# Performance work log

Hardware: AMD Instinct MI355X
Metric: run time of the kernel (lower is better)

The kernel has to match this reference:

```python
import jax, jax.numpy as jnp
import numpy as np
from jax import lax

B, T1, T2, C = 8, 128, 128, 256
K = 3

def setup_inputs() -> dict:
    key = jax.random.key(0)
    k1, k2, kw, kb = jax.random.split(key, 4)
    x1 = jax.random.normal(k1, (B, T1, C), dtype=jnp.float32)
    x2 = jax.random.normal(k2, (B, T2, C), dtype=jnp.float32)
    # conv2d: in_channels = 2C, out_channels = C, kernel 3x3 (OIHW)
    fan_in = 2 * C * K * K
    bound = 1.0 / np.sqrt(fan_in)
    W = jax.random.uniform(kw, (C, 2 * C, K, K), jnp.float32, -bound, bound)
    b = jax.random.uniform(kb, (C,), jnp.float32, -bound, bound)
    alpha = jnp.float32(0.5)
    return {"x1": x1, "x2": x2, "W": W, "b": b, "alpha": alpha}


def reference(x1, x2, W, b, alpha):
    # x1: [B, T1, C], x2: [B, T2, C]
    a = jnp.transpose(x1, (0, 2, 1))  # [B, C, T1]
    c2 = jnp.transpose(x2, (0, 2, 1))  # [B, C, T2]
    Bd, Cd, T1d = a.shape
    T2d = c2.shape[-1]
    # joint outer-product tensor: [B, 2C, T1, T2]
    j1 = jnp.broadcast_to(a[:, :, :, None], (Bd, Cd, T1d, T2d))
    j2 = jnp.broadcast_to(c2[:, :, None, :], (Bd, Cd, T1d, T2d))
    joint = jnp.concatenate([j1, j2], axis=1)
    out = lax.conv_general_dilated(
        joint, W, window_strides=(1, 1), padding="SAME",
        dimension_numbers=("NCHW", "OIHW", "NCHW"))
    out = out + b[None, :, None, None]
    out = jax.nn.gelu(out, approximate=False)  # torch nn.GELU default = exact erf
    out_T1 = jnp.mean(out, axis=-1)            # [B, C, T1]
    out_T1 = jnp.transpose(out_T1, (0, 2, 1))  # [B, T1, C]
    return out_T1 * alpha + x1
```

## Files before the change

### kernel.cpp

```cpp
#include <hip/hip_runtime.h>
#include <math.h>

#define B_   8
#define T_   128
#define C_   256
#define M_   1024
#define NO   2304
#define LDP  136

typedef unsigned short ushort;
typedef ushort ushort8v __attribute__((ext_vector_type(8)));
typedef __bf16 bf16x8  __attribute__((ext_vector_type(8)));
typedef float  f32x4   __attribute__((ext_vector_type(4)));

__device__ __forceinline__ ushort f2bf(float f) {
    unsigned u = __float_as_uint(f);
    u += 0x7fffu + ((u >> 16) & 1u);
    return (ushort)(u >> 16);
}

__device__ __forceinline__ float gelu_fast(float x) {
    float x2 = x * x;
    float y  = x * fmaf(0.0713548162726f, x2, 1.59576912161f);
    float e  = __expf(-y);
    return x * __builtin_amdgcn_rcpf(1.0f + e);
}

__device__ __forceinline__ ushort8v pack8(float4 lo, float4 hi) {
    ushort8v u;
    u[0] = f2bf(lo.x); u[1] = f2bf(lo.y); u[2] = f2bf(lo.z); u[3] = f2bf(lo.w);
    u[4] = f2bf(hi.x); u[5] = f2bf(hi.y); u[6] = f2bf(hi.z); u[7] = f2bf(hi.w);
    return u;
}

__global__ __launch_bounds__(256) void tc_pack_w(
    const float* __restrict__ W, ushort* __restrict__ Wt)
{
    const int o = blockIdx.x, t = threadIdx.x;
    __shared__ ushort lw[4608];
    const float* src = W + (size_t)o * 4608;
    #pragma unroll
    for (int i = 0; i < 18; ++i)
        lw[t + i * 256] = f2bf(src[t + i * 256]);
    __syncthreads();
    #pragma unroll
    for (int i = 0; i < 18; ++i) {
        int e   = t + i * 256;
        int row = e >> 8;
        int c   = e & 255;
        int s   = (row >= 9);
        int r   = row - s * 9;
        Wt[((size_t)s * NO + o * 9 + r) * C_ + c] = lw[((s << 8) + c) * 9 + r];
    }
}

__global__ __launch_bounds__(256) void tc_gemm(
    const float* __restrict__ x1, const float* __restrict__ x2,
    const ushort* __restrict__ Wt, float* __restrict__ G)
{
    const int tn = blockIdx.x;
    const int tm = blockIdx.y;
    const int s  = blockIdx.z;

    __shared__ ushort As[64 * LDP];
    __shared__ ushort Bs[64 * LDP];

    const int tid = threadIdx.x;
    const int r   = tid & 63;
    const int q   = tid >> 6;

    const float*  Xr = (s ? x2 : x1) + ((size_t)(tm * 64 + r)) * C_ + q * 32;
    const ushort* Wr = Wt + ((size_t)s * NO + tn * 64 + r) * C_ + q * 32;

    float4 al0[8], al1[8];
    ushort8v bl0[4], bl1[4];
    #pragma unroll
    for (int i = 0; i < 8; ++i) al0[i] = *(const float4*)(Xr + i * 4);
    #pragma unroll
    for (int i = 0; i < 4; ++i) bl0[i] = *(const ushort8v*)(Wr + i * 8);
    #pragma unroll
    for (int i = 0; i < 8; ++i) al1[i] = *(const float4*)(Xr + 128 + i * 4);
    #pragma unroll
    for (int i = 0; i < 4; ++i) bl1[i] = *(const ushort8v*)(Wr + 128 + i * 8);

    const int st = r * LDP + q * 32;
    #pragma unroll
    for (int c = 0; c < 4; ++c) {
        *(ushort8v*)&As[st + c * 8] = pack8(al0[2 * c], al0[2 * c + 1]);
        *(ushort8v*)&Bs[st + c * 8] = bl0[c];
    }
    __syncthreads();

    const int wr  = q >> 1, wc = q & 1;
    const int r16 = tid & 15, kb = (tid & 63) >> 4;
    const int ar  = (wr * 32 + r16) * LDP + kb * 8;
    const int br  = (wc * 32 + r16) * LDP + kb * 8;

    f32x4 acc[2][2] = {};
    #pragma unroll
    for (int ks = 0; ks < 4; ++ks) {
        bf16x8 a0 = __builtin_bit_cast(bf16x8, *(const ushort8v*)&As[ar + ks * 32]);
        bf16x8 a1 = __builtin_bit_cast(bf16x8, *(const ushort8v*)&As[ar + 16 * LDP + ks * 32]);
        bf16x8 b0 = __builtin_bit_cast(bf16x8, *(const ushort8v*)&Bs[br + ks * 32]);
        bf16x8 b1 = __builtin_bit_cast(bf16x8, *(const ushort8v*)&Bs[br + 16 * LDP + ks * 32]);
        acc[0][0] = __builtin_amdgcn_mfma_f32_16x16x32_bf16(a0, b0, acc[0][0], 0, 0, 0);
        acc[0][1] = __builtin_amdgcn_mfma_f32_16x16x32_bf16(a0, b1, acc[0][1], 0, 0, 0);
        acc[1][0] = __builtin_amdgcn_mfma_f32_16x16x32_bf16(a1, b0, acc[1][0], 0, 0, 0);
        acc[1][1] = __builtin_amdgcn_mfma_f32_16x16x32_bf16(a1, b1, acc[1][1], 0, 0, 0);
    }
    __syncthreads();

    #pragma unroll
    for (int c = 0; c < 4; ++c) {
        *(ushort8v*)&As[st + c * 8] = pack8(al1[2 * c], al1[2 * c + 1]);
        *(ushort8v*)&Bs[st + c * 8] = bl1[c];
    }
    __syncthreads();

    #pragma unroll
    for (int ks = 0; ks < 4; ++ks) {
        bf16x8 a0 = __builtin_bit_cast(bf16x8, *(const ushort8v*)&As[ar + ks * 32]);
        bf16x8 a1 = __builtin_bit_cast(bf16x8, *(const ushort8v*)&As[ar + 16 * LDP + ks * 32]);
        bf16x8 b0 = __builtin_bit_cast(bf16x8, *(const ushort8v*)&Bs[br + ks * 32]);
        bf16x8 b1 = __builtin_bit_cast(bf16x8, *(const ushort8v*)&Bs[br + 16 * LDP + ks * 32]);
        acc[0][0] = __builtin_amdgcn_mfma_f32_16x16x32_bf16(a0, b0, acc[0][0], 0, 0, 0);
        acc[0][1] = __builtin_amdgcn_mfma_f32_16x16x32_bf16(a0, b1, acc[0][1], 0, 0, 0);
        acc[1][0] = __builtin_amdgcn_mfma_f32_16x16x32_bf16(a1, b0, acc[1][0], 0, 0, 0);
        acc[1][1] = __builtin_amdgcn_mfma_f32_16x16x32_bf16(a1, b1, acc[1][1], 0, 0, 0);
    }

    #pragma unroll
    for (int j = 0; j < 2; ++j) {
        int n = tn * 64 + wc * 32 + j * 16 + r16;
        #pragma unroll
        for (int i = 0; i < 2; ++i) {
            int m = tm * 64 + wr * 32 + i * 16 + kb * 4;
            *(f32x4*)&G[((size_t)s * NO + n) * M_ + m] = acc[i][j];
        }
    }
}

__global__ __launch_bounds__(128) void tc_finalize(
    const float* __restrict__ G, const float* __restrict__ x1,
    const float* __restrict__ bias, const float* __restrict__ alpha_p,
    float* __restrict__ out)
{
    const int o = blockIdx.x & 255;
    const int b = blockIdx.x >> 8;
    const int t = threadIdx.x;

    __shared__ float Bs3[T_], BsT[T_], BsB[T_];

    const float* G0 = G + ((size_t)o * 9) * M_ + b * T_;
    const float* G1 = G + ((size_t)NO + o * 9) * M_ + b * T_;

    float a[3] = {0.f, 0.f, 0.f};
    #pragma unroll
    for (int kh = 0; kh < 3; ++kh) {
        int tm = t + kh - 1;
        if (tm >= 0 && tm < T_) {
            #pragma unroll
            for (int kw = 0; kw < 3; ++kw)
                a[kw] += G0[(kh * 3 + kw) * M_ + tm];
        }
    }
    float bb[3] = {0.f, 0.f, 0.f};
    #pragma unroll
    for (int kw = 0; kw < 3; ++kw) {
        int tm = t + kw - 1;
        if (tm >= 0 && tm < T_) {
            #pragma unroll
            for (int kh = 0; kh < 3; ++kh)
                bb[kh] += G1[(kh * 3 + kw) * M_ + tm];
        }
    }

    Bs3[t] = bb[0] + bb[1] + bb[2];
    BsT[t] = bb[1] + bb[2];
    BsB[t] = bb[0] + bb[1];

    float bo = bias[o];
    float A3 = bo + a[0] + a[1] + a[2];
    float Al = bo + a[1] + a[2];
    float Ar = bo + a[0] + a[1];

    __syncthreads();

    const float* Bsel = (t == 0) ? BsT : ((t == T_ - 1) ? BsB : Bs3);

    float s0 = 0.f, s1 = 0.f, s2 = 0.f, s3 = 0.f;
    for (int j = 0; j < T_; j += 4) {
        s0 += gelu_fast(A3 + Bsel[j]);
        s1 += gelu_fast(A3 + Bsel[j + 1]);
        s2 += gelu_fast(A3 + Bsel[j + 2]);
        s3 += gelu_fast(A3 + Bsel[j + 3]);
    }
    float sacc = (s0 + s1) + (s2 + s3);
    sacc += gelu_fast(Al + Bsel[0])      - gelu_fast(A3 + Bsel[0]);
    sacc += gelu_fast(Ar + Bsel[T_ - 1]) - gelu_fast(A3 + Bsel[T_ - 1]);

    float alpha = *alpha_p;
    size_t oi = ((size_t)b * T_ + t) * C_ + o;
    out[oi] = sacc * (alpha * (1.0f / (float)T_)) + x1[oi];
}

extern "C" void kernel_launch(void* const* d_in, const int* in_sizes, int n_in,
                              void* d_out, int out_size, void* d_ws, size_t ws_size,
                              hipStream_t stream) {
    const float* x1    = (const float*)d_in[0];
    const float* x2    = (const float*)d_in[1];
    const float* W     = (const float*)d_in[2];
    const float* bias  = (const float*)d_in[3];
    const float* alpha = (const float*)d_in[4];
    float* out = (float*)d_out;

    float*  G  = (float*)d_ws;
    ushort* Wt = (ushort*)((char*)d_ws + (size_t)2 * NO * M_ * 4);

    tc_pack_w<<<256, 256, 0, stream>>>(W, Wt);
    tc_gemm<<<dim3(NO / 64, M_ / 64, 2), 256, 0, stream>>>(x1, x2, Wt, G);
    tc_finalize<<<B_ * C_, T_, 0, stream>>>(G, x1, bias, alpha, out);
}
```

Baseline: 104.6 us.

## Fuse GEMM and GELU-mean finalize into one kernel, pre-pack inputs to bf16

Replaces the three-kernel pipeline (pack W, GEMM writing a large fp32 G buffer, finalize) with two kernels. The first packs W and converts x1/x2 to bf16. The second runs, per batch and 8-output-channel group, the MFMA GEMM over both halves with register double-buffered loads, stages results as bf16 in LDS, and does the shifted sums, GELU row-mean and residual in place. This removes the global G round trip and one launch, at the cost of storing intermediates in bf16 and a grid of only 256 blocks of 512 threads. GELU now uses exp2 with pre-scaled constants.

```diff
diff --git a/kernel.cpp b/kernel.cpp
--- a/kernel.cpp
+++ b/kernel.cpp
@@ -4,204 +4,242 @@
 #define B_   8
 #define T_   128
 #define C_   256
-#define M_   1024
-#define NO   2304
-#define LDP  136
+#define XLDP 136
+#define SLDP 82
+
+#define OFF_WS 34816
+#define OFF_S1 20992
+#define OFF_BV 41984
+#define OFF_LO 54272
+#define SMEMB  58880
 
 typedef unsigned short ushort;
 typedef ushort ushort8v __attribute__((ext_vector_type(8)));
 typedef __bf16 bf16x8  __attribute__((ext_vector_type(8)));
 typedef float  f32x4   __attribute__((ext_vector_type(4)));
+typedef float  f32x2   __attribute__((ext_vector_type(2)));
 
 __device__ __forceinline__ ushort f2bf(float f) {
     unsigned u = __float_as_uint(f);
     u += 0x7fffu + ((u >> 16) & 1u);
     return (ushort)(u >> 16);
 }
+__device__ __forceinline__ float bf2f(ushort u) {
+    return __uint_as_float((unsigned)u << 16);
+}
 
 __device__ __forceinline__ float gelu_fast(float x) {
     float x2 = x * x;
-    float y  = x * fmaf(0.0713548162726f, x2, 1.59576912161f);
-    float e  = __expf(-y);
+    float y2 = x * fmaf(0.10294324f, x2, 2.3022082f);
+    float e  = exp2f(-y2);
     return x * __builtin_amdgcn_rcpf(1.0f + e);
 }
 
-__device__ __forceinline__ ushort8v pack8(float4 lo, float4 hi) {
-    ushort8v u;
-    u[0] = f2bf(lo.x); u[1] = f2bf(lo.y); u[2] = f2bf(lo.z); u[3] = f2bf(lo.w);
-    u[4] = f2bf(hi.x); u[5] = f2bf(hi.y); u[6] = f2bf(hi.z); u[7] = f2bf(hi.w);
-    return u;
-}
-
-__global__ __launch_bounds__(256) void tc_pack_w(
-    const float* __restrict__ W, ushort* __restrict__ Wt)
+__global__ __launch_bounds__(256) void tc_pack(
+    const float* __restrict__ x1, const float* __restrict__ x2,
+    const float* __restrict__ W, ushort* __restrict__ Xp,
+    ushort* __restrict__ Wt)
 {
-    const int o = blockIdx.x, t = threadIdx.x;
-    __shared__ ushort lw[4608];
-    const float* src = W + (size_t)o * 4608;
-    #pragma unroll
-    for (int i = 0; i < 18; ++i)
-        lw[t + i * 256] = f2bf(src[t + i * 256]);
-    __syncthreads();
-    #pragma unroll
-    for (int i = 0; i < 18; ++i) {
-        int e   = t + i * 256;
-        int row = e >> 8;
-        int c   = e & 255;
-        int s   = (row >= 9);
-        int r   = row - s * 9;
-        Wt[((size_t)s * NO + o * 9 + r) * C_ + c] = lw[((s << 8) + c) * 9 + r];
-    }
-}
-
-__global__ __launch_bounds__(256) void tc_gemm(
-    const float* __restrict__ x1, const float* __restrict__ x2,
-    const ushort* __restrict__ Wt, float* __restrict__ G)
+    const int bid = blockIdx.x, t = threadIdx.x;
+    if (bid < 256) {
+        __shared__ ushort lw[4608];
+        const float* src = W + (size_t)bid * 4608;
+        #pragma unroll
+        for (int i = 0; i < 18; ++i)
+            lw[t + i * 256] = f2bf(src[t + i * 256]);
+        __syncthreads();
+        #pragma unroll
+        for (int i = 0; i < 18; ++i) {
+            int d = t + i * 256;
+            int c = d & 255;
+            int row18 = d >> 8;
+            int s = (row18 >= 9) ? 1 : 0;
+            int r = row18 - s * 9;
+            int rsrc = (s == 0) ? r : ((r % 3) * 3 + (r / 3));
+            Wt[(((size_t)s * 256 + bid) * 9 + r) * 256 + c] = lw[(s * 256 + c) * 9 + rsrc];
+        }
+    } else {
+        int g = (bid - 256) * 256 + t;
+        int e = g * 8;
+        int s  = e >> 18;
+        int me = e & 262143;
+        int m  = me >> 8, c = me & 255;
+        const float* src = (s ? x2 : x1) + (size_t)m * 256 + c;
+        float4 lo = *(const float4*)src;
+        float4 hi = *(const float4*)(src + 4);
+        ushort8v u;
+        u[0] = f2bf(lo.x); u[1] = f2bf(lo.y); u[2] = f2bf(lo.z); u[3] = f2bf(lo.w);
+        u[4] = f2bf(hi.x); u[5] = f2bf(hi.y); u[6] = f2bf(hi.z); u[7] = f2bf(hi.w);
+        *(ushort8v*)&Xp[e] = u;
+    }
+}
+
+__global__ __launch_bounds__(512) void tc_fused(
+    const ushort* __restrict__ Xp, const ushort* __restrict__ Wt,
+    const float* __restrict__ x1, const float* __restrict__ bias,
+    const float* __restrict__ alpha_p, float* __restrict__ out)
 {
-    const int tn = blockIdx.x;
-    const int tm = blockIdx.y;
-    const int s  = blockIdx.z;
-
-    __shared__ ushort As[64 * LDP];
-    __shared__ ushort Bs[64 * LDP];
-
-    const int tid = threadIdx.x;
-    const int r   = tid & 63;
-    const int q   = tid >> 6;
-
-    const float*  Xr = (s ? x2 : x1) + ((size_t)(tm * 64 + r)) * C_ + q * 32;
-    const ushort* Wr = Wt + ((size_t)s * NO + tn * 64 + r) * C_ + q * 32;
-
-    float4 al0[8], al1[8];
-    ushort8v bl0[4], bl1[4];
-    #pragma unroll
-    for (int i = 0; i < 8; ++i) al0[i] = *(const float4*)(Xr + i * 4);
-    #pragma unroll
-    for (int i = 0; i < 4; ++i) bl0[i] = *(const ushort8v*)(Wr + i * 8);
-    #pragma unroll
-    for (int i = 0; i < 8; ++i) al1[i] = *(const float4*)(Xr + 128 + i * 4);
-    #pragma unroll
-    for (int i = 0; i < 4; ++i) bl1[i] = *(const ushort8v*)(Wr + 128 + i * 8);
-
-    const int st = r * LDP + q * 32;
-    #pragma unroll
-    for (int c = 0; c < 4; ++c) {
-        *(ushort8v*)&As[st + c * 8] = pack8(al0[2 * c], al0[2 * c + 1]);
-        *(ushort8v*)&Bs[st + c * 8] = bl0[c];
-    }
-    __syncthreads();
-
-    const int wr  = q >> 1, wc = q & 1;
-    const int r16 = tid & 15, kb = (tid & 63) >> 4;
-    const int ar  = (wr * 32 + r16) * LDP + kb * 8;
-    const int br  = (wc * 32 + r16) * LDP + kb * 8;
-
-    f32x4 acc[2][2] = {};
-    #pragma unroll
-    for (int ks = 0; ks < 4; ++ks) {
-        bf16x8 a0 = __builtin_bit_cast(bf16x8, *(const ushort8v*)&As[ar + ks * 32]);
-        bf16x8 a1 = __builtin_bit_cast(bf16x8, *(const ushort8v*)&As[ar + 16 * LDP + ks * 32]);
-        bf16x8 b0 = __builtin_bit_cast(bf16x8, *(const ushort8v*)&Bs[br + ks * 32]);
-        bf16x8 b1 = __builtin_bit_cast(bf16x8, *(const ushort8v*)&Bs[br + 16 * LDP + ks * 32]);
-        acc[0][0] = __builtin_amdgcn_mfma_f32_16x16x32_bf16(a0, b0, acc[0][0], 0, 0, 0);
-        acc[0][1] = __builtin_amdgcn_mfma_f32_16x16x32_bf16(a0, b1, acc[0][1], 0, 0, 0);
-        acc[1][0] = __builtin_amdgcn_mfma_f32_16x16x32_bf16(a1, b0, acc[1][0], 0, 0, 0);
-        acc[1][1] = __builtin_amdgcn_mfma_f32_16x16x32_bf16(a1, b1, acc[1][1], 0, 0, 0);
-    }
-    __syncthreads();
-
-    #pragma unroll
-    for (int c = 0; c < 4; ++c) {
-        *(ushort8v*)&As[st + c * 8] = pack8(al1[2 * c], al1[2 * c + 1]);
-        *(ushort8v*)&Bs[st + c * 8] = bl1[c];
-    }
-    __syncthreads();
-
-    #pragma unroll
-    for (int ks = 0; ks < 4; ++ks) {
-        bf16x8 a0 = __builtin_bit_cast(bf16x8, *(const ushort8v*)&As[ar + ks * 32]);
-        bf16x8 a1 = __builtin_bit_cast(bf16x8, *(const ushort8v*)&As[ar + 16 * LDP + ks * 32]);
-        bf16x8 b0 = __builtin_bit_cast(bf16x8, *(const ushort8v*)&Bs[br + ks * 32]);
-        bf16x8 b1 = __builtin_bit_cast(bf16x8, *(const ushort8v*)&Bs[br + 16 * LDP + ks * 32]);
-        acc[0][0] = __builtin_amdgcn_mfma_f32_16x16x32_bf16(a0, b0, acc[0][0], 0, 0, 0);
-        acc[0][1] = __builtin_amdgcn_mfma_f32_16x16x32_bf16(a0, b1, acc[0][1], 0, 0, 0);
-        acc[1][0] = __builtin_amdgcn_mfma_f32_16x16x32_bf16(a1, b0, acc[1][0], 0, 0, 0);
-        acc[1][1] = __builtin_amdgcn_mfma_f32_16x16x32_bf16(a1, b1, acc[1][1], 0, 0, 0);
-    }
-
-    #pragma unroll
-    for (int j = 0; j < 2; ++j) {
-        int n = tn * 64 + wc * 32 + j * 16 + r16;
-        #pragma unroll
-        for (int i = 0; i < 2; ++i) {
-            int m = tm * 64 + wr * 32 + i * 16 + kb * 4;
-            *(f32x4*)&G[((size_t)s * NO + n) * M_ + m] = acc[i][j];
-        }
-    }
-}
-
-__global__ __launch_bounds__(128) void tc_finalize(
-    const float* __restrict__ G, const float* __restrict__ x1,
-    const float* __restrict__ bias, const float* __restrict__ alpha_p,
-    float* __restrict__ out)
-{
-    const int o = blockIdx.x & 255;
-    const int b = blockIdx.x >> 8;
-    const int t = threadIdx.x;
-
-    __shared__ float Bs3[T_], BsT[T_], BsB[T_];
-
-    const float* G0 = G + ((size_t)o * 9) * M_ + b * T_;
-    const float* G1 = G + ((size_t)NO + o * 9) * M_ + b * T_;
-
-    float a[3] = {0.f, 0.f, 0.f};
-    #pragma unroll
-    for (int kh = 0; kh < 3; ++kh) {
-        int tm = t + kh - 1;
-        if (tm >= 0 && tm < T_) {
+    __shared__ __align__(16) char smem[SMEMB];
+    ushort* Xs = (ushort*)smem;
+    ushort* Ws = (ushort*)(smem + OFF_WS);
+    float*  Bv = (float*)(smem + OFF_BV);
+    float*  Lo = (float*)(smem + OFF_LO);
+
+    const int u  = threadIdx.x;
+    const int b  = blockIdx.x >> 5;
+    const int og = blockIdx.x & 31;
+    const int l  = u & 63, w = u >> 6;
+    const int r16 = l & 15, kb = l >> 4;
+
+    const int xrow = u >> 2, xcb = (u & 3) * 32;
+    const ushort* Xrow0 = Xp + ((size_t)(b * T_ + xrow)) * C_ + xcb;
+    const ushort* WtB   = Wt + ((size_t)og * 72) * C_;
+
+    f32x4 acc[2][5] = {};
+    ushort8v xbuf[2][4];
+    ushort8v wbuf[2][3];
+
+    #pragma unroll
+    for (int c4 = 0; c4 < 4; ++c4) xbuf[0][c4] = *(const ushort8v*)(Xrow0 + c4 * 8);
+    {
+        int c0 = u;          int r0 = c0 >> 4, o0 = (c0 & 15) * 8;
+        int c1 = 512 + u;    int r1 = c1 >> 4, o1 = (c1 & 15) * 8;
+        wbuf[0][0] = *(const ushort8v*)(WtB + (size_t)r0 * C_ + o0);
+        wbuf[0][1] = *(const ushort8v*)(WtB + (size_t)r1 * C_ + o1);
+        if (u < 128) {
+            int c2 = 1024 + u; int r2 = c2 >> 4, o2 = (c2 & 15) * 8;
+            wbuf[0][2] = *(const ushort8v*)(WtB + (size_t)r2 * C_ + o2);
+        }
+    }
+
+    #pragma unroll
+    for (int r = 0; r < 4; ++r) {
+        const int cur = r & 1;
+        __syncthreads();
+        #pragma unroll
+        for (int c4 = 0; c4 < 4; ++c4)
+            *(ushort8v*)&Xs[xrow * XLDP + xcb + c4 * 8] = xbuf[cur][c4];
+        {
+            int c0 = u;       *(ushort8v*)&Ws[(c0 >> 4) * XLDP + (c0 & 15) * 8] = wbuf[cur][0];
+            int c1 = 512 + u; *(ushort8v*)&Ws[(c1 >> 4) * XLDP + (c1 & 15) * 8] = wbuf[cur][1];
+            if (u < 128) {
+                int c2 = 1024 + u;
+                *(ushort8v*)&Ws[(c2 >> 4) * XLDP + (c2 & 15) * 8] = wbuf[cur][2];
+            }
+        }
+        if (r < 3) {
+            const int rn = r + 1, sn = rn >> 1, pn = rn & 1;
+            const ushort* xsrc = Xrow0 + (size_t)sn * 262144 + pn * 128;
             #pragma unroll
-            for (int kw = 0; kw < 3; ++kw)
-                a[kw] += G0[(kh * 3 + kw) * M_ + tm];
-        }
-    }
-    float bb[3] = {0.f, 0.f, 0.f};
-    #pragma unroll
-    for (int kw = 0; kw < 3; ++kw) {
-        int tm = t + kw - 1;
-        if (tm >= 0 && tm < T_) {
+            for (int c4 = 0; c4 < 4; ++c4)
+                xbuf[cur ^ 1][c4] = *(const ushort8v*)(xsrc + c4 * 8);
+            const ushort* wsrc = WtB + (size_t)sn * 2304 * C_ + pn * 128;
+            int c0 = u;       wbuf[cur ^ 1][0] = *(const ushort8v*)(wsrc + (size_t)(c0 >> 4) * C_ + (c0 & 15) * 8);
+            int c1 = 512 + u; wbuf[cur ^ 1][1] = *(const ushort8v*)(wsrc + (size_t)(c1 >> 4) * C_ + (c1 & 15) * 8);
+            if (u < 128) {
+                int c2 = 1024 + u;
+                wbuf[cur ^ 1][2] = *(const ushort8v*)(wsrc + (size_t)(c2 >> 4) * C_ + (c2 & 15) * 8);
+            }
+        }
+        __syncthreads();
+        const int s = r >> 1;
+        #pragma unroll
+        for (int ks = 0; ks < 4; ++ks) {
+            bf16x8 af = __builtin_bit_cast(bf16x8,
+                *(const ushort8v*)&Xs[(w * 16 + r16) * XLDP + ks * 32 + kb * 8]);
             #pragma unroll
-            for (int kh = 0; kh < 3; ++kh)
-                bb[kh] += G1[(kh * 3 + kw) * M_ + tm];
-        }
-    }
-
-    Bs3[t] = bb[0] + bb[1] + bb[2];
-    BsT[t] = bb[1] + bb[2];
-    BsB[t] = bb[0] + bb[1];
-
-    float bo = bias[o];
-    float A3 = bo + a[0] + a[1] + a[2];
-    float Al = bo + a[1] + a[2];
-    float Ar = bo + a[0] + a[1];
-
-    __syncthreads();
-
-    const float* Bsel = (t == 0) ? BsT : ((t == T_ - 1) ? BsB : Bs3);
-
-    float s0 = 0.f, s1 = 0.f, s2 = 0.f, s3 = 0.f;
-    for (int j = 0; j < T_; j += 4) {
-        s0 += gelu_fast(A3 + Bsel[j]);
-        s1 += gelu_fast(A3 + Bsel[j + 1]);
-        s2 += gelu_fast(A3 + Bsel[j + 2]);
-        s3 += gelu_fast(A3 + Bsel[j + 3]);
-    }
-    float sacc = (s0 + s1) + (s2 + s3);
-    sacc += gelu_fast(Al + Bsel[0])      - gelu_fast(A3 + Bsel[0]);
-    sacc += gelu_fast(Ar + Bsel[T_ - 1]) - gelu_fast(A3 + Bsel[T_ - 1]);
-
-    float alpha = *alpha_p;
-    size_t oi = ((size_t)b * T_ + t) * C_ + o;
-    out[oi] = sacc * (alpha * (1.0f / (float)T_)) + x1[oi];
+            for (int nf = 0; nf < 5; ++nf) {
+                bf16x8 bf = __builtin_bit_cast(bf16x8,
+                    *(const ushort8v*)&Ws[(nf * 16 + r16) * XLDP + ks * 32 + kb * 8]);
+                acc[s][nf] = __builtin_amdgcn_mfma_f32_16x16x32_bf16(af, bf, acc[s][nf], 0, 0, 0);
+            }
+        }
+    }
+    __syncthreads();
+
+    #pragma unroll
+    for (int s = 0; s < 2; ++s) {
+        ushort* Sb = (ushort*)(smem + (s ? OFF_S1 : 0));
+        #pragma unroll
+        for (int nf = 0; nf < 5; ++nf) {
+            int n = nf * 16 + r16;
+            if (n < 72) {
+                #pragma unroll
+                for (int reg = 0; reg < 4; ++reg) {
+                    int m = w * 16 + kb * 4 + reg;
+                    Sb[m * SLDP + n] = f2bf(acc[s][nf][reg]);
+                }
+            }
+        }
+    }
+    __syncthreads();
+
+    const int oo  = w;
+    const int t0  = l;
+    const int o_g = og * 8 + oo;
+    const float bo = bias[o_g];
+    const ushort* S0 = (const ushort*)smem;
+    const ushort* S1 = (const ushort*)(smem + OFF_S1);
+    float A3[2], Al[2], Ar[2];
+    #pragma unroll
+    for (int idx = 0; idx < 2; ++idx) {
+        int tt = t0 + idx * 64;
+        float a0 = 0.f, a1 = 0.f, a2 = 0.f;
+        #pragma unroll
+        for (int sh = 0; sh < 3; ++sh) {
+            int row = tt + sh - 1;
+            if (row >= 0 && row < T_) {
+                int base = row * SLDP + oo * 9 + sh * 3;
+                a0 += bf2f(S0[base]); a1 += bf2f(S0[base + 1]); a2 += bf2f(S0[base + 2]);
+            }
+        }
+        A3[idx] = bo + a0 + a1 + a2;
+        Al[idx] = bo + a1 + a2;
+        Ar[idx] = bo + a0 + a1;
+        float b0 = 0.f, b1 = 0.f, b2 = 0.f;
+        #pragma unroll
+        for (int sh = 0; sh < 3; ++sh) {
+            int row = tt + sh - 1;
+            if (row >= 0 && row < T_) {
+                int base = row * SLDP + oo * 9 + sh * 3;
+                b0 += bf2f(S1[base]); b1 += bf2f(S1[base + 1]); b2 += bf2f(S1[base + 2]);
+            }
+        }
+        Bv[(oo * 3 + 0) * T_ + tt] = b0 + b1 + b2;
+        Bv[(oo * 3 + 1) * T_ + tt] = b1 + b2;
+        Bv[(oo * 3 + 2) * T_ + tt] = b0 + b1;
+    }
+    __syncthreads();
+
+    #pragma unroll
+    for (int idx = 0; idx < 2; ++idx) {
+        int tt  = t0 + idx * 64;
+        int cls = (tt == 0) ? 1 : ((tt == T_ - 1) ? 2 : 0);
+        const float* Bs = Bv + (oo * 3 + cls) * T_;
+        float A = A3[idx];
+        float s0 = 0.f, s1 = 0.f, s2 = 0.f, s3 = 0.f;
+        for (int j = 0; j < T_; j += 4) {
+            f32x4 v = *(const f32x4*)&Bs[j];
+            s0 += gelu_fast(A + v[0]); s1 += gelu_fast(A + v[1]);
+            s2 += gelu_fast(A + v[2]); s3 += gelu_fast(A + v[3]);
+        }
+        float sm = (s0 + s1) + (s2 + s3);
+        float bl = Bs[0], br = Bs[T_ - 1];
+        sm += gelu_fast(Al[idx] + bl) - gelu_fast(A + bl);
+        sm += gelu_fast(Ar[idx] + br) - gelu_fast(A + br);
+        Lo[tt * 9 + oo] = sm;
+    }
+    __syncthreads();
+
+    const float kk = (*alpha_p) * (1.0f / (float)T_);
+    {
+        int row = u >> 2, c2 = (u & 3) * 2;
+        size_t go = ((size_t)(b * T_ + row)) * C_ + og * 8 + c2;
+        f32x2 r;
+        r[0] = Lo[row * 9 + c2]     * kk + x1[go];
+        r[1] = Lo[row * 9 + c2 + 1] * kk + x1[go + 1];
+        *(f32x2*)&out[go] = r;
+    }
 }
 
 extern "C" void kernel_launch(void* const* d_in, const int* in_sizes, int n_in,
@@ -214,10 +252,9 @@
     const float* alpha = (const float*)d_in[4];
     float* out = (float*)d_out;
 
-    float*  G  = (float*)d_ws;
-    ushort* Wt = (ushort*)((char*)d_ws + (size_t)2 * NO * M_ * 4);
-
-    tc_pack_w<<<256, 256, 0, stream>>>(W, Wt);
-    tc_gemm<<<dim3(NO / 64, M_ / 64, 2), 256, 0, stream>>>(x1, x2, Wt, G);
-    tc_finalize<<<B_ * C_, T_, 0, stream>>>(G, x1, bias, alpha, out);
-}
+    ushort* Xp = (ushort*)d_ws;
+    ushort* Wt = Xp + (size_t)2 * 1024 * 256;
+
+    tc_pack<<<512, 256, 0, stream>>>(x1, x2, W, Xp, Wt);
+    tc_fused<<<256, 512, 0, stream>>>(Xp, Wt, x1, bias, alpha, out);
+}
```

Result: faster. 91.46 us (-12.6%).
